# Performance work log

Measured on AMD Instinct MI355X. Metric: run time of the kernel, lower is better.

Reference implementation:

```python
import jax, jax.numpy as jnp
import numpy as np


def setup_inputs() -> dict:
    key = jax.random.key(0)
    k1, k2, k3 = jax.random.split(key, 3)
    B, T, D, U = 64, 1024, 256, 512
    inputs = jax.random.normal(k1, (B, T, D), dtype=jnp.float32)
    W_xh = jax.random.normal(k2, (D, U), dtype=jnp.float32) * (1.0 / np.sqrt(D))
    W_hh = jax.random.normal(k3, (U, U), dtype=jnp.float32) * (1.0 / np.sqrt(U))
    b_h = jnp.zeros((U,), dtype=jnp.float32)
    return {"inputs": inputs, "W_xh": W_xh, "W_hh": W_hh, "b_h": b_h}


def reference(inputs, W_xh, W_hh, b_h):
    # h_t = tanh(x_t @ W_xh + h_{t-1} @ W_hh + b_h); return_sequences=True
    B, T, D = inputs.shape
    U = W_hh.shape[0]
    # input projection is time-independent: precompute once (same math)
    xw = jnp.einsum('btd,du->btu', inputs, W_xh) + b_h  # (B, T, U)
    h0 = jnp.zeros((B, U), dtype=inputs.dtype)

    def step(h_prev, xw_t):
        h_t = jnp.tanh(xw_t + h_prev @ W_hh)
        return h_t, h_t

    _, hs = jax.lax.scan(step, h0, jnp.swapaxes(xw, 0, 1))  # (T, B, U)
    return jnp.swapaxes(hs, 0, 1)  # (B, T, U)
```

## Files before the change

kernel.cpp:

```cpp
#include <hip/hip_runtime.h>


typedef __attribute__((ext_vector_type(8))) short short8;
typedef __attribute__((ext_vector_type(4))) float f32x4;

#define T_SZ 1024
#define U_SZ 512

typedef union { unsigned long long q[2]; short8 v; } chunk16;

__device__ __forceinline__ unsigned short f2bf(float f){
  unsigned u = __float_as_uint(f);
  u += 0x7FFFu + ((u >> 16) & 1u);
  return (unsigned short)(u >> 16);
}
__device__ __forceinline__ float bf2f(unsigned short s){
  return __uint_as_float(((unsigned)s) << 16);
}

__global__ __launch_bounds__(256) void xw_gemm(const float* __restrict__ X,
                                               const float* __restrict__ W,
                                               const float* __restrict__ bias,
                                               float* __restrict__ out){
  __shared__ float As[16][132];
  __shared__ float Bs[16][68];
  const int tid = threadIdx.x;
  const int tx = tid & 15, ty = tid >> 4;
  const int row0 = blockIdx.x * 128;
  const int col0 = blockIdx.y * 64;
  float acc[8][4];
  #pragma unroll
  for(int a=0;a<8;a++)
    #pragma unroll
    for(int b=0;b<4;b++) acc[a][b]=0.f;

  for(int kc=0;kc<256;kc+=16){
    {
      const int m  = tid >> 2;
      const int kq = (tid & 3) * 4;
      #pragma unroll
      for(int h=0;h<2;h++){
        const float4 v = *(const float4*)&X[(size_t)(row0 + m + 64*h)*256 + kc + kq];
        As[kq+0][m+64*h]=v.x; As[kq+1][m+64*h]=v.y;
        As[kq+2][m+64*h]=v.z; As[kq+3][m+64*h]=v.w;
      }
    }
    {
      const int k = tid >> 4;
      const int c = (tid & 15) * 4;
      *(float4*)&Bs[k][c] = *(const float4*)&W[(size_t)(kc + k)*512 + col0 + c];
    }
    __syncthreads();
    #pragma unroll
    for(int k=0;k<16;k++){
      const float4 b4 = *(const float4*)&Bs[k][tx*4];
      const float4 a0 = *(const float4*)&As[k][ty*8];
      const float4 a1 = *(const float4*)&As[k][ty*8+4];
      const float av[8] = {a0.x,a0.y,a0.z,a0.w,a1.x,a1.y,a1.z,a1.w};
      const float bv[4] = {b4.x,b4.y,b4.z,b4.w};
      #pragma unroll
      for(int ii=0;ii<8;ii++)
        #pragma unroll
        for(int j=0;j<4;j++) acc[ii][j] = fmaf(av[ii], bv[j], acc[ii][j]);
    }
    __syncthreads();
  }
  #pragma unroll
  for(int ii=0;ii<8;ii++){
    const int row = row0 + ty*8 + ii;
    float4 o;
    o.x = acc[ii][0] + bias[col0+tx*4+0];
    o.y = acc[ii][1] + bias[col0+tx*4+1];
    o.z = acc[ii][2] + bias[col0+tx*4+2];
    o.w = acc[ii][3] + bias[col0+tx*4+3];
    *(float4*)&out[(size_t)row*512 + col0 + tx*4] = o;
  }
}

__global__ __launch_bounds__(512, 2) void rnn_rec(const float* __restrict__ Whh,
                                                  float* __restrict__ out,
                                                  int* __restrict__ flags,
                                                  unsigned short* __restrict__ ring){
  __shared__ unsigned short Ahi[2][16][520];
  __shared__ unsigned short Alo[2][16][520];

  const int bid = blockIdx.x;
  const int g  = bid & 3;
  const int i  = bid >> 2;
  const int tid = threadIdx.x;
  const int lane = tid & 63;
  const int w  = tid >> 6;
  const int ln = lane & 15;
  const int lq = lane >> 4;
  const int b0 = g * 16;
  const int ncol0 = i*128 + w*16;

  short8 whi[16], wlo[16];
  #pragma unroll
  for(int kt=0;kt<16;kt++){
    short8 h8, l8;
    const int kb = kt*32 + lq*8;
    #pragma unroll
    for(int j=0;j<8;j++){
      const float wv = Whh[(size_t)(kb+j)*U_SZ + ncol0 + ln];
      const unsigned short hb = f2bf(wv);
      const unsigned short lb = f2bf(wv - bf2f(hb));
      h8[j] = (short)hb; l8[j] = (short)lb;
    }
    whi[kt]=h8; wlo[kt]=l8;
  }
  for(int idx=tid; idx<2*16*520; idx+=512){
    ((unsigned short*)Ahi)[idx]=0;
    ((unsigned short*)Alo)[idx]=0;
  }
  __syncthreads();

  float xwv[4], hprev[4];
  #pragma unroll
  for(int r=0;r<4;r++){
    xwv[r] = out[((size_t)(b0 + lq*4 + r)*T_SZ + 0)*U_SZ + ncol0 + ln];
    hprev[r] = 0.f;
  }

  const int selp = lane >> 5;
  const int mrow = (lane & 31) >> 1;
  const int qh   = lane & 1;

  for(int t=0;t<T_SZ;t++){
    const int buf = t & 1;
    if(t>0){
      #pragma unroll
      for(int r=0;r<4;r++)
        out[((size_t)(b0 + lq*4 + r)*T_SZ + (t-1))*U_SZ + ncol0 + ln] = hprev[r];
      {
        const int p = lane + (lane >= i);
        bool done = (lane >= 3);
        while(__ballot(!done)){
          if(!done){
            const int f = __hip_atomic_load(&flags[((g*4+p)*8 + w)*32],
                                            __ATOMIC_RELAXED, __HIP_MEMORY_SCOPE_AGENT);
            done = (f >= t);
          }
        }
      }
      asm volatile("" ::: "memory");
      const size_t slot = (size_t)((t-1)&1);
      #pragma unroll
      for(int s=0;s<3;s++){
        const int p = s + (s >= i);
        const unsigned long long* rb = (const unsigned long long*)ring
            + (((slot*4 + g)*4 + p)*8 + w)*128 + selp*64 + mrow*4 + qh*2;
        chunk16 cc;
        cc.q[0] = __hip_atomic_load(rb+0, __ATOMIC_RELAXED, __HIP_MEMORY_SCOPE_AGENT);
        cc.q[1] = __hip_atomic_load(rb+1, __ATOMIC_RELAXED, __HIP_MEMORY_SCOPE_AGENT);
        unsigned short* dst = selp ? &Alo[buf][mrow][p*128 + w*16 + qh*8]
                                   : &Ahi[buf][mrow][p*128 + w*16 + qh*8];
        *(short8*)dst = cc.v;
      }
    }
    __syncthreads();

    f32x4 c_hh = {0.f,0.f,0.f,0.f}, c_hl = {0.f,0.f,0.f,0.f}, c_lh = {0.f,0.f,0.f,0.f};
    #pragma unroll
    for(int kt=0;kt<16;kt++){
      const int k = kt*32 + lq*8;
      const short8 ah = *(const short8*)&Ahi[buf][ln][k];
      const short8 al = *(const short8*)&Alo[buf][ln][k];
      c_hh = __builtin_amdgcn_mfma_f32_16x16x32_bf16(ah, whi[kt], c_hh, 0, 0, 0);
      c_hl = __builtin_amdgcn_mfma_f32_16x16x32_bf16(ah, wlo[kt], c_hl, 0, 0, 0);
      c_lh = __builtin_amdgcn_mfma_f32_16x16x32_bf16(al, whi[kt], c_lh, 0, 0, 0);
    }
    const f32x4 csum = c_hh + c_hl + c_lh;
    const int nbuf = buf ^ 1;
    #pragma unroll
    for(int r=0;r<4;r++){
      float pre = csum[r] + xwv[r];
      pre = fminf(fmaxf(pre, -12.f), 12.f);
      const float e = __expf(2.f*pre);
      const float h = (e-1.f)/(e+1.f);
      hprev[r] = h;
      const unsigned short hb = f2bf(h);
      const unsigned short lb = f2bf(h - bf2f(hb));
      Ahi[nbuf][lq*4+r][ncol0+ln] = hb;
      Alo[nbuf][lq*4+r][ncol0+ln] = lb;
    }
    {
      const unsigned short* src = selp ? &Alo[nbuf][mrow][ncol0 + qh*8]
                                       : &Ahi[nbuf][mrow][ncol0 + qh*8];
      chunk16 ck; ck.v = *(const short8*)src;
      unsigned long long* rb = (unsigned long long*)ring
          + ((((size_t)(t&1)*4 + g)*4 + i)*8 + w)*128 + selp*64 + mrow*4 + qh*2;
      __hip_atomic_store(rb+0, ck.q[0], __ATOMIC_RELAXED, __HIP_MEMORY_SCOPE_AGENT);
      __hip_atomic_store(rb+1, ck.q[1], __ATOMIC_RELAXED, __HIP_MEMORY_SCOPE_AGENT);
    }
    asm volatile("s_waitcnt vmcnt(0)" ::: "memory");
    if(lane==0)
      __hip_atomic_store(&flags[((g*4+i)*8 + w)*32], t+1,
                         __ATOMIC_RELAXED, __HIP_MEMORY_SCOPE_AGENT);
    {
      const int tn = (t < T_SZ-1) ? t+1 : t;
      #pragma unroll
      for(int r=0;r<4;r++)
        xwv[r] = out[((size_t)(b0 + lq*4 + r)*T_SZ + tn)*U_SZ + ncol0 + ln];
    }
  }
  #pragma unroll
  for(int r=0;r<4;r++)
    out[((size_t)(b0 + lq*4 + r)*T_SZ + (T_SZ-1))*U_SZ + ncol0 + ln] = hprev[r];
}

extern "C" void kernel_launch(void* const* d_in, const int* in_sizes, int n_in,
                              void* d_out, int out_size, void* d_ws, size_t ws_size,
                              hipStream_t stream) {
  (void)in_sizes; (void)n_in; (void)out_size; (void)ws_size;
  const float* X   = (const float*)d_in[0];
  const float* Wxh = (const float*)d_in[1];
  const float* Whh = (const float*)d_in[2];
  const float* bh  = (const float*)d_in[3];
  float* out = (float*)d_out;

  int* flags = (int*)d_ws;
  unsigned short* ring = (unsigned short*)((char*)d_ws + 16384);

  xw_gemm<<<dim3(512, 8), 256, 0, stream>>>(X, Wxh, bh, out);
  rnn_rec<<<16, 512, 0, stream>>>(Whh, out, flags, ring);
}
```

Before: 3.674 ms.

## Embed step tags in ring payload words to replace separate flag synchronization

Measured after the change: 4.047 ms. 10.1% more time.

```diff
diff --git a/kernel.cpp b/kernel.cpp
--- a/kernel.cpp
+++ b/kernel.cpp
@@ -79,8 +79,7 @@
 
 __global__ __launch_bounds__(512, 2) void rnn_rec(const float* __restrict__ Whh,
                                                   float* __restrict__ out,
-                                                  int* __restrict__ flags,
-                                                  unsigned short* __restrict__ ring){
+                                                  unsigned long long* __restrict__ ringq){
   __shared__ unsigned short Ahi[2][16][520];
   __shared__ unsigned short Alo[2][16][520];
 
@@ -126,36 +125,46 @@
   const int mrow = (lane & 31) >> 1;
   const int qh   = lane & 1;
 
+  int peer[3];
+  #pragma unroll
+  for(int s=0;s<3;s++) peer[s] = s + (s >= i);
+
   for(int t=0;t<T_SZ;t++){
     const int buf = t & 1;
     if(t>0){
       #pragma unroll
       for(int r=0;r<4;r++)
         out[((size_t)(b0 + lq*4 + r)*T_SZ + (t-1))*U_SZ + ncol0 + ln] = hprev[r];
-      {
-        const int p = lane + (lane >= i);
-        bool done = (lane >= 3);
-        while(__ballot(!done)){
-          if(!done){
-            const int f = __hip_atomic_load(&flags[((g*4+p)*8 + w)*32],
-                                            __ATOMIC_RELAXED, __HIP_MEMORY_SCOPE_AGENT);
-            done = (f >= t);
+      const size_t slot = (size_t)((t-1)&1);
+      int rem = 7;
+      while(__ballot(rem != 0)){
+        if(rem){
+          unsigned long long wv[3][3];
+          #pragma unroll
+          for(int s=0;s<3;s++) if(rem & (1<<s)){
+            const unsigned long long* rb = ringq
+                + (((slot*4 + g)*4 + peer[s])*8 + w)*192 + lane*3;
+            wv[s][0] = __hip_atomic_load(rb+0, __ATOMIC_RELAXED, __HIP_MEMORY_SCOPE_AGENT);
+            wv[s][1] = __hip_atomic_load(rb+1, __ATOMIC_RELAXED, __HIP_MEMORY_SCOPE_AGENT);
+            wv[s][2] = __hip_atomic_load(rb+2, __ATOMIC_RELAXED, __HIP_MEMORY_SCOPE_AGENT);
+          }
+          #pragma unroll
+          for(int s=0;s<3;s++) if(rem & (1<<s)){
+            const unsigned e0 = (unsigned)(wv[s][0] >> 48);
+            const unsigned e1 = (unsigned)(wv[s][1] >> 48);
+            const unsigned e2 = (unsigned)(wv[s][2] >> 48);
+            if((e0 == (unsigned)t) & (e1 == (unsigned)t) & (e2 == (unsigned)t)){
+              chunk16 cc;
+              cc.q[0] = (wv[s][0] & 0x0000FFFFFFFFFFFFull) | (wv[s][1] << 48);
+              cc.q[1] = ((wv[s][1] >> 16) & 0xFFFFFFFFull) | (wv[s][2] << 32);
+              const int p = peer[s];
+              unsigned short* dst = selp ? &Alo[buf][mrow][p*128 + w*16 + qh*8]
+                                         : &Ahi[buf][mrow][p*128 + w*16 + qh*8];
+              *(short8*)dst = cc.v;
+              rem &= ~(1<<s);
+            }
           }
         }
-      }
-      asm volatile("" ::: "memory");
-      const size_t slot = (size_t)((t-1)&1);
-      #pragma unroll
-      for(int s=0;s<3;s++){
-        const int p = s + (s >= i);
-        const unsigned long long* rb = (const unsigned long long*)ring
-            + (((slot*4 + g)*4 + p)*8 + w)*128 + selp*64 + mrow*4 + qh*2;
-        chunk16 cc;
-        cc.q[0] = __hip_atomic_load(rb+0, __ATOMIC_RELAXED, __HIP_MEMORY_SCOPE_AGENT);
-        cc.q[1] = __hip_atomic_load(rb+1, __ATOMIC_RELAXED, __HIP_MEMORY_SCOPE_AGENT);
-        unsigned short* dst = selp ? &Alo[buf][mrow][p*128 + w*16 + qh*8]
-                                   : &Ahi[buf][mrow][p*128 + w*16 + qh*8];
-        *(short8*)dst = cc.v;
       }
     }
     __syncthreads();
@@ -188,15 +197,17 @@
       const unsigned short* src = selp ? &Alo[nbuf][mrow][ncol0 + qh*8]
                                        : &Ahi[nbuf][mrow][ncol0 + qh*8];
       chunk16 ck; ck.v = *(const short8*)src;
-      unsigned long long* rb = (unsigned long long*)ring
-          + ((((size_t)(t&1)*4 + g)*4 + i)*8 + w)*128 + selp*64 + mrow*4 + qh*2;
-      __hip_atomic_store(rb+0, ck.q[0], __ATOMIC_RELAXED, __HIP_MEMORY_SCOPE_AGENT);
-      __hip_atomic_store(rb+1, ck.q[1], __ATOMIC_RELAXED, __HIP_MEMORY_SCOPE_AGENT);
-    }
-    asm volatile("s_waitcnt vmcnt(0)" ::: "memory");
-    if(lane==0)
-      __hip_atomic_store(&flags[((g*4+i)*8 + w)*32], t+1,
-                         __ATOMIC_RELAXED, __HIP_MEMORY_SCOPE_AGENT);
+      const unsigned long long E = (unsigned long long)(t+1) << 48;
+      const unsigned long long o0 = (ck.q[0] & 0x0000FFFFFFFFFFFFull) | E;
+      const unsigned long long o1 = (((ck.q[0] >> 48) | (ck.q[1] << 16))
+                                     & 0x0000FFFFFFFFFFFFull) | E;
+      const unsigned long long o2 = (ck.q[1] >> 32) | E;
+      unsigned long long* rb = ringq
+          + ((((size_t)(t&1)*4 + g)*4 + i)*8 + w)*192 + lane*3;
+      __hip_atomic_store(rb+0, o0, __ATOMIC_RELAXED, __HIP_MEMORY_SCOPE_AGENT);
+      __hip_atomic_store(rb+1, o1, __ATOMIC_RELAXED, __HIP_MEMORY_SCOPE_AGENT);
+      __hip_atomic_store(rb+2, o2, __ATOMIC_RELAXED, __HIP_MEMORY_SCOPE_AGENT);
+    }
     {
       const int tn = (t < T_SZ-1) ? t+1 : t;
       #pragma unroll
@@ -219,9 +230,10 @@
   const float* bh  = (const float*)d_in[3];
   float* out = (float*)d_out;
 
-  int* flags = (int*)d_ws;
-  unsigned short* ring = (unsigned short*)((char*)d_ws + 16384);
+  unsigned long long* ringq = (unsigned long long*)d_ws;
+  const size_t ring_bytes = 2ull*4*4*8*192*8;
 
   xw_gemm<<<dim3(512, 8), 256, 0, stream>>>(X, Wxh, bh, out);
-  rnn_rec<<<16, 512, 0, stream>>>(Whh, out, flags, ring);
-}
+  hipMemsetAsync(d_ws, 0, ring_bytes, stream);
+  rnn_rec<<<16, 512, 0, stream>>>(Whh, out, ringq);
+}
```
